# Optimization experiments

Hardware: AMD Instinct MI355X
Metric: run time of the kernel (lower is better)

Reference implementation:

```python
import jax, jax.numpy as jnp
import numpy as np

B, DIM, HID, K, G, MID = 1024, 384, 64, 8, 48, 128
EPS = 1e-06


def _gaussian_8x8():
    t = jnp.arange(K, dtype=jnp.float32) - 3.5
    g = jnp.exp(-(t[:, None] ** 2 + t[None, :] ** 2) / (2.0 * 2.0 ** 2))
    return g / g.sum()


def setup_inputs() -> dict:
    key = jax.random.key(0)
    ks = jax.random.split(key, 16)
    inp = {
        "x": jax.random.normal(ks[0], (B, DIM), dtype=jnp.float32),
        "W": jax.random.normal(ks[1], (DIM, HID), dtype=jnp.float32) * 0.02,
        "b": jax.random.normal(ks[2], (DIM, HID), dtype=jnp.float32) * 0.02,
        "patch_weight": _gaussian_8x8(),  # learnable 8x8, softmaxed in forward
        "pair_w1": jax.random.normal(ks[3], (G, G), dtype=jnp.float32) * 0.02,
        "pair_b1": jax.random.normal(ks[4], (G, G), dtype=jnp.float32) * 0.02,
        "pair_w2": jax.random.normal(ks[5], (G, G), dtype=jnp.float32) * 0.02,
        "pair_b2": jax.random.normal(ks[6], (G, G), dtype=jnp.float32) * 0.02,
        # nn.Linear(G, DIM)
        "proj_w": jax.random.normal(ks[7], (DIM, G), dtype=jnp.float32) * (1.0 / np.sqrt(G)),
        "proj_b": jax.random.normal(ks[8], (DIM,), dtype=jnp.float32) * 0.02,
        # nn.Linear(HID, MID)
        "down_w": jax.random.normal(ks[9], (MID, HID), dtype=jnp.float32) * (1.0 / np.sqrt(HID)),
        "down_b": jax.random.normal(ks[10], (MID,), dtype=jnp.float32) * 0.02,
        # nn.Linear(MID, HID)
        "up_w": jax.random.normal(ks[11], (HID, MID), dtype=jnp.float32) * (1.0 / np.sqrt(MID)),
        "up_b": jax.random.normal(ks[12], (HID,), dtype=jnp.float32) * 0.02,
    }
    return inp


def _leaky(v):
    return jnp.where(v >= 0, v, 0.01 * v)


def reference(x, W, b, patch_weight, pair_w1, pair_b1, pair_w2, pair_b2,
              proj_w, proj_b, down_w, down_b, up_w, up_b):
    # scale / inverse-bias GELU features: (B, DIM, HID)
    s = x[:, :, None]
    inv = 1.0 / (jnp.abs(s) + EPS)
    H = jax.nn.gelu(s * W[None] + inv * b[None], approximate=False)
    # Gram matrix over hidden dim: (B, DIM, DIM)
    P = jnp.einsum('bik,bjk->bij', H, H)
    # learnable gaussian patch pooling (softmax over flattened 8x8 weights)
    w = jax.nn.softmax(patch_weight.reshape(-1)).reshape(K, K)
    Pg = jnp.einsum('bgkhl,kl->bgh', P.reshape(-1, G, K, G, K), w)  # (B, G, G)
    # two elementwise gated leaky layers
    Pg = _leaky(Pg * pair_w1[None] + pair_b1[None])
    Pg = _leaky(Pg * pair_w2[None] + pair_b2[None])
    # softmax + nonlinear row reduction -> (B, G)
    row_soft = jax.nn.softmax(Pg, axis=-1)
    row_weights = (1.0 / (1.0 + row_soft ** 2)).sum(axis=-1)
    # project 48 -> 384, scale rows of H
    scales = row_weights @ proj_w.T + proj_b  # (B, DIM)
    H = H * scales[:, :, None]
    # tiny MLP on hidden dim
    z = _leaky(H @ down_w.T + down_b)
    z = _leaky(z @ up_w.T + up_b)
    return z
```

## Files before the change

### kernel.cpp

```cpp
#include <hip/hip_runtime.h>


#define EPSF 1e-6f

typedef __attribute__((ext_vector_type(8))) short bf16x8;
typedef __attribute__((ext_vector_type(4))) float f32x4;
typedef __attribute__((ext_vector_type(4))) unsigned short u16x4;

__device__ __forceinline__ unsigned short f2bf(float f) {
    union { float f; unsigned int u; } v; v.f = f;
    unsigned int r = v.u + 0x7fffu + ((v.u >> 16) & 1u);
    return (unsigned short)(r >> 16);
}
__device__ __forceinline__ float bf2f(unsigned short h) {
    union { unsigned int u; float f; } v; v.u = ((unsigned int)h) << 16;
    return v.f;
}
__device__ __forceinline__ float leaky(float v) { return fmaxf(v, 0.01f * v); }
__device__ __forceinline__ int key8(int r) { return (r ^ (r >> 3)) & 7; }
__device__ __forceinline__ float gelu_f(float u) {
    float t = u * (1.5957691216f + 0.0713548163f * (u * u));
    float e = __expf(t);
    float r = __builtin_amdgcn_rcpf(e + 1.0f);
    return fmaf(-u, r, u);
}

__global__ void prep(const float* __restrict__ proj_w,
                     const float* __restrict__ down_w,
                     const float* __restrict__ up_w,
                     float* __restrict__ ws) {
    int idx = blockIdx.x * blockDim.x + threadIdx.x;
    unsigned short* wb = (unsigned short*)(ws + 18432);
    if (idx < 18432) {
        int i = idx / 48, g = idx % 48;
        ws[g * 384 + i] = proj_w[idx];
    } else if (idx < 26624) {
        int k = idx - 18432;
        wb[k] = f2bf(down_w[k]);
    } else if (idx < 34816) {
        int k = idx - 26624;
        wb[8192 + k] = f2bf(up_w[k]);
    }
}

__global__ __launch_bounds__(1024, 4) void fused_main(
    const float* __restrict__ x,
    const float* __restrict__ W,
    const float* __restrict__ bb,
    const float* __restrict__ patch_weight,
    const float* __restrict__ pw1, const float* __restrict__ pb1,
    const float* __restrict__ pw2, const float* __restrict__ pb2,
    const float* __restrict__ proj_b,
    const float* __restrict__ down_b,
    const float* __restrict__ up_b,
    const float* __restrict__ ws,
    float* __restrict__ out)
{
    __shared__ __align__(16) unsigned short sH[24576];
    __shared__ __align__(16) unsigned short sRB[24576];
    __shared__ __align__(16) unsigned short sZ1[24576];
    __shared__ float sw[64];
    __shared__ float srw[48];
    __shared__ float sScale[384];
    __shared__ float sDb[128];
    __shared__ float sUb[64];

    const int t = threadIdx.x;
    const int b = blockIdx.x;
    const int wv = t >> 6, lane = t & 63, q = lane >> 4, r = lane & 15;
    const float* projT = ws;
    const unsigned short* dwB = (const unsigned short*)(ws + 18432);
    const unsigned short* uwB = dwB + 8192;
    unsigned short* sM  = sRB;
    unsigned short* sDW = sRB;
    unsigned short* sUW = sRB + 8192;
    float* sPg = (float*)(sRB + 16384);

    if (t < 64) {
        float p = patch_weight[t];
        float m = p;
        for (int o = 32; o > 0; o >>= 1) m = fmaxf(m, __shfl_xor(m, o));
        float e = __expf(p - m);
        float s = e;
        for (int o = 32; o > 0; o >>= 1) s += __shfl_xor(s, o);
        sw[t] = e * __builtin_amdgcn_rcpf(s);
    }

    for (int j = 0; j < 6; ++j) {
        int idx4 = j * 1024 + t;
        int base = idx4 * 4;
        int i = base >> 6, c0 = base & 63;
        float4 w4 = ((const float4*)W)[idx4];
        float4 b4 = ((const float4*)bb)[idx4];
        float xi  = x[b * 384 + i];
        float inv = __builtin_amdgcn_rcpf(fabsf(xi) + EPSF);
        u16x4 hv;
        hv[0] = f2bf(gelu_f(fmaf(xi, w4.x, inv * b4.x)));
        hv[1] = f2bf(gelu_f(fmaf(xi, w4.y, inv * b4.y)));
        hv[2] = f2bf(gelu_f(fmaf(xi, w4.z, inv * b4.z)));
        hv[3] = f2bf(gelu_f(fmaf(xi, w4.w, inv * b4.w)));
        int cb = c0 >> 3, cc = c0 & 7;
        *(u16x4*)&sH[i * 64 + ((cb ^ key8(i)) << 3) + cc] = hv;
    }
    __syncthreads();

    if (t < 768) {
        const int cb = t & 7, lq = (t >> 3) & 1, g = t >> 4;
        float acc[4][8];
        #pragma unroll
        for (int a = 0; a < 4; ++a)
            #pragma unroll
            for (int cc = 0; cc < 8; ++cc) acc[a][cc] = 0.0f;
        #pragma unroll
        for (int k = 0; k < 8; ++k) {
            int i = g * 8 + k;
            bf16x8 hv = *(const bf16x8*)&sH[i * 64 + ((cb ^ key8(i)) << 3)];
            f32x4 w4 = *(const f32x4*)&sw[k * 8 + lq * 4];
            float hf[8];
            #pragma unroll
            for (int cc = 0; cc < 8; ++cc) hf[cc] = bf2f((unsigned short)hv[cc]);
            #pragma unroll
            for (int a = 0; a < 4; ++a)
                #pragma unroll
                for (int cc = 0; cc < 8; ++cc) acc[a][cc] = fmaf(w4[a], hf[cc], acc[a][cc]);
        }
        #pragma unroll
        for (int a = 0; a < 4; ++a) {
            int l = lq * 4 + a;
            bf16x8 mv;
            #pragma unroll
            for (int cc = 0; cc < 8; ++cc) mv[cc] = (short)f2bf(acc[a][cc]);
            *(bf16x8*)&sM[g * 512 + ((l * 8 + (cb ^ key8(g))) << 3)] = mv;
        }
    }
    __syncthreads();

    f32x4 pacc = {0.f, 0.f, 0.f, 0.f};
    if (wv < 9) {
        const int tg = wv / 3, th = wv % 3;
        for (int ks = 0; ks < 16; ++ks) {
            int kf = ks * 32 + q * 8;
            int g = tg * 16 + r;
            int cbg = kf >> 3;
            int cbs = (cbg & ~7) | ((cbg ^ key8(g)) & 7);
            bf16x8 av = *(const bf16x8*)&sM[g * 512 + (cbs << 3)];
            int h = th * 16 + r;
            int i = h * 8 + (kf >> 6);
            int cbh = (kf & 63) >> 3;
            bf16x8 bv = *(const bf16x8*)&sH[i * 64 + ((cbh ^ key8(i)) << 3)];
            pacc = __builtin_amdgcn_mfma_f32_16x16x32_bf16(av, bv, pacc, 0, 0, 0);
        }
        #pragma unroll
        for (int reg = 0; reg < 4; ++reg) {
            int g = tg * 16 + q * 4 + reg;
            int h = th * 16 + r;
            int idx = g * 48 + h;
            float v = pacc[reg];
            v = leaky(fmaf(v, pw1[idx], pb1[idx]));
            v = leaky(fmaf(v, pw2[idx], pb2[idx]));
            pacc[reg] = v;
        }
    }
    __syncthreads();

    if (wv < 9) {
        const int tg = wv / 3, th = wv % 3;
        #pragma unroll
        for (int reg = 0; reg < 4; ++reg) {
            int g = tg * 16 + q * 4 + reg;
            int h = th * 16 + r;
            sPg[g * 49 + h] = pacc[reg];
        }
    } else {
        for (int cid = t - 576; cid < 2048; cid += 448) {
            if (cid < 1024) {
                int nrow = cid >> 3, cb = cid & 7;
                bf16x8 v = *(const bf16x8*)&dwB[cid * 8];
                *(bf16x8*)&sDW[nrow * 64 + ((cb ^ key8(nrow)) << 3)] = v;
            } else {
                int c2 = cid - 1024;
                int rrow = c2 >> 4, cb = c2 & 15;
                bf16x8 v = *(const bf16x8*)&uwB[c2 * 8];
                int cbs = (cb & 8) | ((cb ^ key8(rrow)) & 7);
                *(bf16x8*)&sUW[rrow * 128 + (cbs << 3)] = v;
            }
        }
    }
    if (t < 128) sDb[t] = down_b[t];
    else if (t < 192) sUb[t - 128] = up_b[t - 128];
    __syncthreads();

    {
        #pragma unroll
        for (int rr = 0; rr < 3; ++rr) {
            int row = wv + rr * 16;
            float v = (lane < 48) ? sPg[row * 49 + lane] : -1e30f;
            float m = v;
            for (int o = 32; o > 0; o >>= 1) m = fmaxf(m, __shfl_xor(m, o));
            float e = (lane < 48) ? __expf(v - m) : 0.0f;
            float s = e;
            for (int o = 32; o > 0; o >>= 1) s += __shfl_xor(s, o);
            float p = e * __builtin_amdgcn_rcpf(s);
            float rwv = (lane < 48) ? __builtin_amdgcn_rcpf(fmaf(p, p, 1.0f)) : 0.0f;
            for (int o = 32; o > 0; o >>= 1) rwv += __shfl_xor(rwv, o);
            if (lane == 0) srw[row] = rwv;
        }
    }
    __syncthreads();

    if (t < 384) {
        float s = proj_b[t];
        #pragma unroll 4
        for (int g = 0; g < 48; ++g) s = fmaf(srw[g], projT[g * 384 + t], s);
        sScale[t] = s;
    }
    __syncthreads();

    const int mg = wv >> 2, ng = wv & 3;
    for (int rt = 0; rt < 2; ++rt) {
        const int r0 = rt * 192;
        {
            f32x4 zacc[3][2];
            #pragma unroll
            for (int a = 0; a < 3; ++a)
                #pragma unroll
                for (int e = 0; e < 2; ++e) zacc[a][e] = (f32x4){0.f, 0.f, 0.f, 0.f};
            #pragma unroll
            for (int ks = 0; ks < 2; ++ks) {
                int cb = ks * 4 + q;
                bf16x8 af[3];
                #pragma unroll
                for (int a = 0; a < 3; ++a) {
                    int i = r0 + (mg * 3 + a) * 16 + r;
                    af[a] = *(const bf16x8*)&sH[i * 64 + ((cb ^ key8(i)) << 3)];
                }
                #pragma unroll
                for (int e = 0; e < 2; ++e) {
                    int n = (ng * 2 + e) * 16 + r;
                    bf16x8 bv = *(const bf16x8*)&sDW[n * 64 + ((cb ^ key8(n)) << 3)];
                    #pragma unroll
                    for (int a = 0; a < 3; ++a)
                        zacc[a][e] = __builtin_amdgcn_mfma_f32_16x16x32_bf16(af[a], bv, zacc[a][e], 0, 0, 0);
                }
            }
            #pragma unroll
            for (int a = 0; a < 3; ++a) {
                #pragma unroll
                for (int e = 0; e < 2; ++e) {
                    #pragma unroll
                    for (int reg = 0; reg < 4; ++reg) {
                        int rl = (mg * 3 + a) * 16 + q * 4 + reg;
                        int m = (ng * 2 + e) * 16 + r;
                        float v = leaky(fmaf(zacc[a][e][reg], sScale[r0 + rl], sDb[m]));
                        int cb2 = m >> 3;
                        int cbs2 = (cb2 & 8) | ((cb2 ^ key8(rl)) & 7);
                        sZ1[rl * 128 + (cbs2 << 3) + (m & 7)] = f2bf(v);
                    }
                }
            }
        }
        __syncthreads();
        {
            f32x4 oacc[3];
            #pragma unroll
            for (int a = 0; a < 3; ++a) oacc[a] = (f32x4){0.f, 0.f, 0.f, 0.f};
            #pragma unroll
            for (int ks = 0; ks < 4; ++ks) {
                int cb = ks * 4 + q;
                int cp = ng * 16 + r;
                int cbsB = (cb & 8) | ((cb ^ key8(cp)) & 7);
                bf16x8 bv = *(const bf16x8*)&sUW[cp * 128 + (cbsB << 3)];
                #pragma unroll
                for (int a = 0; a < 3; ++a) {
                    int rl = (mg * 3 + a) * 16 + r;
                    int cbsA = (cb & 8) | ((cb ^ key8(rl)) & 7);
                    bf16x8 av = *(const bf16x8*)&sZ1[rl * 128 + (cbsA << 3)];
                    oacc[a] = __builtin_amdgcn_mfma_f32_16x16x32_bf16(av, bv, oacc[a], 0, 0, 0);
                }
            }
            #pragma unroll
            for (int a = 0; a < 3; ++a) {
                #pragma unroll
                for (int reg = 0; reg < 4; ++reg) {
                    int i = r0 + (mg * 3 + a) * 16 + q * 4 + reg;
                    int cp = ng * 16 + r;
                    out[(b * 384 + i) * 64 + cp] = leaky(oacc[a][reg] + sUb[cp]);
                }
            }
        }
        __syncthreads();
    }
}

extern "C" void kernel_launch(void* const* d_in, const int* in_sizes, int n_in,
                              void* d_out, int out_size, void* d_ws, size_t ws_size,
                              hipStream_t stream) {
    const float* x      = (const float*)d_in[0];
    const float* W      = (const float*)d_in[1];
    const float* bb     = (const float*)d_in[2];
    const float* pw     = (const float*)d_in[3];
    const float* pw1    = (const float*)d_in[4];
    const float* pb1    = (const float*)d_in[5];
    const float* pw2    = (const float*)d_in[6];
    const float* pb2    = (const float*)d_in[7];
    const float* proj_w = (const float*)d_in[8];
    const float* proj_b = (const float*)d_in[9];
    const float* down_w = (const float*)d_in[10];
    const float* down_b = (const float*)d_in[11];
    const float* up_w   = (const float*)d_in[12];
    const float* up_b   = (const float*)d_in[13];
    float* out = (float*)d_out;
    float* ws  = (float*)d_ws;

    prep<<<(34816 + 255) / 256, 256, 0, stream>>>(proj_w, down_w, up_w, ws);
    fused_main<<<1024, 1024, 0, stream>>>(x, W, bb, pw, pw1, pb1, pw2, pb2,
                                          proj_b, down_b, up_b, ws, out);
}
```

Before: 199.2 us.

## Shrink shared memory footprint to raise occupancy and stream MLP weights from global

Cuts LDS use from about 144KB to about 72KB by splitting the patch-pooled matrix into two hidden-dim halves and by dropping the LDS copies of the down/up weights, which are now read directly from global/L2. The MLP stage is retiled into four 96-row chunks, and launch bounds are raised to allow more blocks per CU. The aim is to let a second block co-reside per CU so one block's phases overlap with another's. The cost is extra barriers, repeated global weight loads, and tighter register limits.

```diff
diff --git a/kernel.cpp b/kernel.cpp
--- a/kernel.cpp
+++ b/kernel.cpp
@@ -43,7 +43,7 @@
     }
 }
 
-__global__ __launch_bounds__(1024, 4) void fused_main(
+__global__ __launch_bounds__(1024, 8) void fused_main(
     const float* __restrict__ x,
     const float* __restrict__ W,
     const float* __restrict__ bb,
@@ -57,8 +57,7 @@
     float* __restrict__ out)
 {
     __shared__ __align__(16) unsigned short sH[24576];
-    __shared__ __align__(16) unsigned short sRB[24576];
-    __shared__ __align__(16) unsigned short sZ1[24576];
+    __shared__ __align__(16) unsigned short sRB[12288];
     __shared__ float sw[64];
     __shared__ float srw[48];
     __shared__ float sScale[384];
@@ -72,9 +71,8 @@
     const unsigned short* dwB = (const unsigned short*)(ws + 18432);
     const unsigned short* uwB = dwB + 8192;
     unsigned short* sM  = sRB;
-    unsigned short* sDW = sRB;
-    unsigned short* sUW = sRB + 8192;
-    float* sPg = (float*)(sRB + 16384);
+    float* sPg = (float*)sRB;
+    unsigned short* sZ1 = sRB;
 
     if (t < 64) {
         float p = patch_weight[t];
@@ -104,52 +102,62 @@
     }
     __syncthreads();
 
-    if (t < 768) {
-        const int cb = t & 7, lq = (t >> 3) & 1, g = t >> 4;
-        float acc[4][8];
-        #pragma unroll
-        for (int a = 0; a < 4; ++a)
-            #pragma unroll
-            for (int cc = 0; cc < 8; ++cc) acc[a][cc] = 0.0f;
-        #pragma unroll
-        for (int k = 0; k < 8; ++k) {
-            int i = g * 8 + k;
-            bf16x8 hv = *(const bf16x8*)&sH[i * 64 + ((cb ^ key8(i)) << 3)];
-            f32x4 w4 = *(const f32x4*)&sw[k * 8 + lq * 4];
-            float hf[8];
-            #pragma unroll
-            for (int cc = 0; cc < 8; ++cc) hf[cc] = bf2f((unsigned short)hv[cc]);
-            #pragma unroll
-            for (int a = 0; a < 4; ++a)
-                #pragma unroll
-                for (int cc = 0; cc < 8; ++cc) acc[a][cc] = fmaf(w4[a], hf[cc], acc[a][cc]);
-        }
-        #pragma unroll
-        for (int a = 0; a < 4; ++a) {
-            int l = lq * 4 + a;
-            bf16x8 mv;
-            #pragma unroll
-            for (int cc = 0; cc < 8; ++cc) mv[cc] = (short)f2bf(acc[a][cc]);
-            *(bf16x8*)&sM[g * 512 + ((l * 8 + (cb ^ key8(g))) << 3)] = mv;
-        }
-    }
-    __syncthreads();
-
     f32x4 pacc = {0.f, 0.f, 0.f, 0.f};
+    for (int hc = 0; hc < 2; ++hc) {
+        if (t < 768) {
+            const int cb = t & 3, lp = (t >> 2) & 3, g = t >> 4;
+            float acc[2][8];
+            #pragma unroll
+            for (int dl = 0; dl < 2; ++dl)
+                #pragma unroll
+                for (int cc = 0; cc < 8; ++cc) acc[dl][cc] = 0.0f;
+            #pragma unroll
+            for (int k = 0; k < 8; ++k) {
+                int i = g * 8 + k;
+                int cbh = hc * 4 + cb;
+                bf16x8 hv = *(const bf16x8*)&sH[i * 64 + ((cbh ^ key8(i)) << 3)];
+                float w0 = sw[k * 8 + lp * 2];
+                float w1 = sw[k * 8 + lp * 2 + 1];
+                float hf[8];
+                #pragma unroll
+                for (int cc = 0; cc < 8; ++cc) hf[cc] = bf2f((unsigned short)hv[cc]);
+                #pragma unroll
+                for (int cc = 0; cc < 8; ++cc) {
+                    acc[0][cc] = fmaf(w0, hf[cc], acc[0][cc]);
+                    acc[1][cc] = fmaf(w1, hf[cc], acc[1][cc]);
+                }
+            }
+            #pragma unroll
+            for (int dl = 0; dl < 2; ++dl) {
+                int l = lp * 2 + dl;
+                int cbl = l * 4 + cb;
+                int cbs = (cbl & 24) | ((cbl ^ key8(g)) & 7);
+                bf16x8 mv;
+                #pragma unroll
+                for (int cc = 0; cc < 8; ++cc) mv[cc] = (short)f2bf(acc[dl][cc]);
+                *(bf16x8*)&sM[g * 256 + (cbs << 3)] = mv;
+            }
+        }
+        __syncthreads();
+        if (wv < 9) {
+            const int tg = wv / 3, th = wv % 3;
+            #pragma unroll
+            for (int ks = 0; ks < 8; ++ks) {
+                int g = tg * 16 + r;
+                int cbl = ks * 4 + q;
+                int cbs = (cbl & 24) | ((cbl ^ key8(g)) & 7);
+                bf16x8 av = *(const bf16x8*)&sM[g * 256 + (cbs << 3)];
+                int i = (th * 16 + r) * 8 + ks;
+                int cbh = hc * 4 + q;
+                bf16x8 bv = *(const bf16x8*)&sH[i * 64 + ((cbh ^ key8(i)) << 3)];
+                pacc = __builtin_amdgcn_mfma_f32_16x16x32_bf16(av, bv, pacc, 0, 0, 0);
+            }
+        }
+        __syncthreads();
+    }
+
     if (wv < 9) {
         const int tg = wv / 3, th = wv % 3;
-        for (int ks = 0; ks < 16; ++ks) {
-            int kf = ks * 32 + q * 8;
-            int g = tg * 16 + r;
-            int cbg = kf >> 3;
-            int cbs = (cbg & ~7) | ((cbg ^ key8(g)) & 7);
-            bf16x8 av = *(const bf16x8*)&sM[g * 512 + (cbs << 3)];
-            int h = th * 16 + r;
-            int i = h * 8 + (kf >> 6);
-            int cbh = (kf & 63) >> 3;
-            bf16x8 bv = *(const bf16x8*)&sH[i * 64 + ((cbh ^ key8(i)) << 3)];
-            pacc = __builtin_amdgcn_mfma_f32_16x16x32_bf16(av, bv, pacc, 0, 0, 0);
-        }
         #pragma unroll
         for (int reg = 0; reg < 4; ++reg) {
             int g = tg * 16 + q * 4 + reg;
@@ -158,137 +166,97 @@
             float v = pacc[reg];
             v = leaky(fmaf(v, pw1[idx], pb1[idx]));
             v = leaky(fmaf(v, pw2[idx], pb2[idx]));
-            pacc[reg] = v;
-        }
-    }
-    __syncthreads();
-
-    if (wv < 9) {
-        const int tg = wv / 3, th = wv % 3;
-        #pragma unroll
-        for (int reg = 0; reg < 4; ++reg) {
-            int g = tg * 16 + q * 4 + reg;
-            int h = th * 16 + r;
-            sPg[g * 49 + h] = pacc[reg];
-        }
-    } else {
-        for (int cid = t - 576; cid < 2048; cid += 448) {
-            if (cid < 1024) {
-                int nrow = cid >> 3, cb = cid & 7;
-                bf16x8 v = *(const bf16x8*)&dwB[cid * 8];
-                *(bf16x8*)&sDW[nrow * 64 + ((cb ^ key8(nrow)) << 3)] = v;
-            } else {
-                int c2 = cid - 1024;
-                int rrow = c2 >> 4, cb = c2 & 15;
-                bf16x8 v = *(const bf16x8*)&uwB[c2 * 8];
-                int cbs = (cb & 8) | ((cb ^ key8(rrow)) & 7);
-                *(bf16x8*)&sUW[rrow * 128 + (cbs << 3)] = v;
-            }
+            sPg[g * 49 + h] = v;
         }
     }
     if (t < 128) sDb[t] = down_b[t];
     else if (t < 192) sUb[t - 128] = up_b[t - 128];
     __syncthreads();
 
-    {
-        #pragma unroll
-        for (int rr = 0; rr < 3; ++rr) {
-            int row = wv + rr * 16;
-            float v = (lane < 48) ? sPg[row * 49 + lane] : -1e30f;
-            float m = v;
-            for (int o = 32; o > 0; o >>= 1) m = fmaxf(m, __shfl_xor(m, o));
-            float e = (lane < 48) ? __expf(v - m) : 0.0f;
-            float s = e;
-            for (int o = 32; o > 0; o >>= 1) s += __shfl_xor(s, o);
-            float p = e * __builtin_amdgcn_rcpf(s);
-            float rwv = (lane < 48) ? __builtin_amdgcn_rcpf(fmaf(p, p, 1.0f)) : 0.0f;
-            for (int o = 32; o > 0; o >>= 1) rwv += __shfl_xor(rwv, o);
-            if (lane == 0) srw[row] = rwv;
-        }
+    if (wv < 12) {
+        int row = wv * 4 + (lane >> 4);
+        int idx = lane & 15;
+        const float* pr = &sPg[row * 49 + idx * 3];
+        float v0 = pr[0], v1 = pr[1], v2 = pr[2];
+        float m = fmaxf(v0, fmaxf(v1, v2));
+        #pragma unroll
+        for (int o = 8; o > 0; o >>= 1) m = fmaxf(m, __shfl_xor(m, o));
+        float e0 = __expf(v0 - m), e1 = __expf(v1 - m), e2 = __expf(v2 - m);
+        float s = e0 + e1 + e2;
+        #pragma unroll
+        for (int o = 8; o > 0; o >>= 1) s += __shfl_xor(s, o);
+        float rs = __builtin_amdgcn_rcpf(s);
+        float p0 = e0 * rs, p1 = e1 * rs, p2 = e2 * rs;
+        float rw = __builtin_amdgcn_rcpf(fmaf(p0, p0, 1.0f))
+                 + __builtin_amdgcn_rcpf(fmaf(p1, p1, 1.0f))
+                 + __builtin_amdgcn_rcpf(fmaf(p2, p2, 1.0f));
+        #pragma unroll
+        for (int o = 8; o > 0; o >>= 1) rw += __shfl_xor(rw, o);
+        if (idx == 0) srw[row] = rw;
     }
     __syncthreads();
 
-    if (t < 384) {
-        float s = proj_b[t];
-        #pragma unroll 4
-        for (int g = 0; g < 48; ++g) s = fmaf(srw[g], projT[g * 384 + t], s);
-        sScale[t] = s;
-    }
-    __syncthreads();
-
-    const int mg = wv >> 2, ng = wv & 3;
-    for (int rt = 0; rt < 2; ++rt) {
-        const int r0 = rt * 192;
-        {
-            f32x4 zacc[3][2];
-            #pragma unroll
-            for (int a = 0; a < 3; ++a)
-                #pragma unroll
-                for (int e = 0; e < 2; ++e) zacc[a][e] = (f32x4){0.f, 0.f, 0.f, 0.f};
-            #pragma unroll
-            for (int ks = 0; ks < 2; ++ks) {
-                int cb = ks * 4 + q;
-                bf16x8 af[3];
-                #pragma unroll
-                for (int a = 0; a < 3; ++a) {
-                    int i = r0 + (mg * 3 + a) * 16 + r;
-                    af[a] = *(const bf16x8*)&sH[i * 64 + ((cb ^ key8(i)) << 3)];
-                }
-                #pragma unroll
-                for (int e = 0; e < 2; ++e) {
-                    int n = (ng * 2 + e) * 16 + r;
-                    bf16x8 bv = *(const bf16x8*)&sDW[n * 64 + ((cb ^ key8(n)) << 3)];
-                    #pragma unroll
-                    for (int a = 0; a < 3; ++a)
-                        zacc[a][e] = __builtin_amdgcn_mfma_f32_16x16x32_bf16(af[a], bv, zacc[a][e], 0, 0, 0);
-                }
-            }
+    const int mg = wv >> 3, ng = wv & 7;
+    #pragma unroll 1
+    for (int rt = 0; rt < 4; ++rt) {
+        const int r0 = rt * 96;
+        if (rt == 0 && t < 384) {
+            float s = proj_b[t];
+            #pragma unroll 4
+            for (int g = 0; g < 48; ++g) s = fmaf(srw[g], projT[g * 384 + t], s);
+            sScale[t] = s;
+        }
+        f32x4 zacc[3];
+        #pragma unroll
+        for (int a = 0; a < 3; ++a) zacc[a] = (f32x4){0.f, 0.f, 0.f, 0.f};
+        #pragma unroll
+        for (int ks = 0; ks < 2; ++ks) {
+            int cb = ks * 4 + q;
+            int n = ng * 16 + r;
+            bf16x8 bv = *(const bf16x8*)&dwB[n * 64 + cb * 8];
             #pragma unroll
             for (int a = 0; a < 3; ++a) {
-                #pragma unroll
-                for (int e = 0; e < 2; ++e) {
-                    #pragma unroll
-                    for (int reg = 0; reg < 4; ++reg) {
-                        int rl = (mg * 3 + a) * 16 + q * 4 + reg;
-                        int m = (ng * 2 + e) * 16 + r;
-                        float v = leaky(fmaf(zacc[a][e][reg], sScale[r0 + rl], sDb[m]));
-                        int cb2 = m >> 3;
-                        int cbs2 = (cb2 & 8) | ((cb2 ^ key8(rl)) & 7);
-                        sZ1[rl * 128 + (cbs2 << 3) + (m & 7)] = f2bf(v);
-                    }
-                }
-            }
-        }
-        __syncthreads();
-        {
-            f32x4 oacc[3];
-            #pragma unroll
-            for (int a = 0; a < 3; ++a) oacc[a] = (f32x4){0.f, 0.f, 0.f, 0.f};
+                int i = r0 + (mg * 3 + a) * 16 + r;
+                bf16x8 av = *(const bf16x8*)&sH[i * 64 + ((cb ^ key8(i)) << 3)];
+                zacc[a] = __builtin_amdgcn_mfma_f32_16x16x32_bf16(av, bv, zacc[a], 0, 0, 0);
+            }
+        }
+        __syncthreads();
+        #pragma unroll
+        for (int a = 0; a < 3; ++a) {
+            #pragma unroll
+            for (int reg = 0; reg < 4; ++reg) {
+                int rl = (mg * 3 + a) * 16 + q * 4 + reg;
+                int m = ng * 16 + r;
+                float v = leaky(fmaf(zacc[a][reg], sScale[r0 + rl], sDb[m]));
+                int cb2 = m >> 3;
+                int cbs2 = (cb2 & 8) | ((cb2 ^ key8(rl)) & 7);
+                sZ1[rl * 128 + (cbs2 << 3) + (m & 7)] = f2bf(v);
+            }
+        }
+        __syncthreads();
+        int ntl = (wv < 8) ? 2 : 1;
+        for (int tt = 0; tt < ntl; ++tt) {
+            int tau = wv + tt * 16;
+            int mt = tau >> 2, nt = tau & 3;
+            f32x4 oacc = {0.f, 0.f, 0.f, 0.f};
             #pragma unroll
             for (int ks = 0; ks < 4; ++ks) {
                 int cb = ks * 4 + q;
-                int cp = ng * 16 + r;
-                int cbsB = (cb & 8) | ((cb ^ key8(cp)) & 7);
-                bf16x8 bv = *(const bf16x8*)&sUW[cp * 128 + (cbsB << 3)];
-                #pragma unroll
-                for (int a = 0; a < 3; ++a) {
-                    int rl = (mg * 3 + a) * 16 + r;
-                    int cbsA = (cb & 8) | ((cb ^ key8(rl)) & 7);
-                    bf16x8 av = *(const bf16x8*)&sZ1[rl * 128 + (cbsA << 3)];
-                    oacc[a] = __builtin_amdgcn_mfma_f32_16x16x32_bf16(av, bv, oacc[a], 0, 0, 0);
-                }
-            }
-            #pragma unroll
-            for (int a = 0; a < 3; ++a) {
-                #pragma unroll
-                for (int reg = 0; reg < 4; ++reg) {
-                    int i = r0 + (mg * 3 + a) * 16 + q * 4 + reg;
-                    int cp = ng * 16 + r;
-                    out[(b * 384 + i) * 64 + cp] = leaky(oacc[a][reg] + sUb[cp]);
-                }
-            }
-        }
-        __syncthreads();
+                int p = nt * 16 + r;
+                bf16x8 bv = *(const bf16x8*)&uwB[p * 128 + cb * 8];
+                int rl = mt * 16 + r;
+                int cbsA = (cb & 8) | ((cb ^ key8(rl)) & 7);
+                bf16x8 av = *(const bf16x8*)&sZ1[rl * 128 + (cbsA << 3)];
+                oacc = __builtin_amdgcn_mfma_f32_16x16x32_bf16(av, bv, oacc, 0, 0, 0);
+            }
+            #pragma unroll
+            for (int reg = 0; reg < 4; ++reg) {
+                int i = r0 + mt * 16 + q * 4 + reg;
+                int cp = nt * 16 + r;
+                out[(b * 384 + i) * 64 + cp] = leaky(oacc[reg] + sUb[cp]);
+            }
+        }
     }
 }
 
```

After: 301.0 us. 51.1% more time.
